# Kernel tuning notes

Hardware: AMD Instinct MI355X
Metric: run time of the kernel (lower is better)

Reference implementation:

```python
import jax, jax.numpy as jnp
import numpy as np

N, E = 20000, 320000
IN_DIM = OUT_DIM = E_IN = E_OUT = 128
BN_EPS = 1e-5

def _lrelu(x):
    return jnp.where(x >= 0, x, 0.1 * x)

def setup_inputs() -> dict:
    key = jax.random.key(0)
    ks = jax.random.split(key, 12)
    def w(k, shape):
        return jax.random.normal(k, shape, jnp.float32) * (shape[0] ** -0.5)
    return {
        "h": jax.random.normal(ks[0], (N, IN_DIM), jnp.float32),
        "edge_w": jax.random.normal(ks[1], (E, E_IN), jnp.float32),
        "W_node": w(ks[2], (IN_DIM, OUT_DIM)),
        "W_eedge": w(ks[3], (E_IN, E_IN)),
        "W_esf": w(ks[4], (E_IN, 1)),
        "W_fuse": w(ks[5], (2 * OUT_DIM + E_IN, OUT_DIM)),
        "b_fuse": jnp.zeros((OUT_DIM,), jnp.float32),
        "W_attn": w(ks[6], (OUT_DIM, 1)),
        "W_conc": w(ks[7], (2 * OUT_DIM + E_IN, OUT_DIM)),
        "b_conc": jnp.zeros((OUT_DIM,), jnp.float32),
        "bn_gamma": jnp.ones((E_IN,), jnp.float32),
        "bn_beta": jnp.zeros((E_IN,), jnp.float32),
        "W_aggre": w(ks[8], (2 * OUT_DIM + 2 * E_IN, E_OUT)),
        "src": jax.random.randint(ks[9], (E,), 0, N),
        "dst": jax.random.randint(ks[10], (E,), 0, N),
    }

def reference(h, edge_w, W_node, W_eedge, W_esf, W_fuse, b_fuse, W_attn,
              W_conc, b_conc, bn_gamma, bn_beta, W_aggre, src, dst):
    # eval mode: dropout = identity, BatchNorm uses running stats (mean 0, var 1)
    hn = h @ W_node                       # embed_node -> ndata['h'] = ndata['oh']
    # self_attention: ow = embed_edge(w); w = edge_sf_atten(lrelu(ow)) * ow
    ow = edge_w @ W_eedge                 # [E, e_in]
    w1 = (_lrelu(ow) @ W_esf) * ow        # [E, e_in]
    # inter_attention
    hs, hd = hn[src], hn[dst]             # [E, out]
    sat = jnp.concatenate([hs, hd, w1], axis=-1)          # [E, 2*out+e_in]
    inw = _lrelu(sat @ W_fuse + b_fuse)                   # [E, out]
    a = inw @ W_attn                                      # [E, 1]
    w2 = a * w1                                           # edata['w']
    # reduce_func2: segment softmax over incoming edges (grouped by dst)
    s = a[:, 0]
    m = jax.ops.segment_max(s, dst, num_segments=N)
    e = jnp.exp(s - m[dst])
    denom = jax.ops.segment_sum(e, dst, num_segments=N)
    alpha = (e / denom[dst])[:, None]                     # [E, 1]
    t = jnp.concatenate([hs, w2], axis=-1)                # [E, out+e_in]
    h_agg = jax.ops.segment_sum(alpha * t, dst, num_segments=N)  # [N, out+e_in]
    h_new = jnp.concatenate([h_agg, hn], axis=-1) @ W_conc + b_conc
    # DGL only updates nodes that received messages; zero-indegree keep embed_node(h)
    indeg = jax.ops.segment_sum(jnp.ones((E,), jnp.float32), dst, num_segments=N)
    h_out = jnp.where(indeg[:, None] > 0, h_new, hn)      # [N, out]
    # edge_calc: BN(w2) then aggre_embed_edge(cat(src_h, dst_h, bn_w, ow))
    w_bn = (w2 / jnp.sqrt(jnp.float32(1.0) + BN_EPS)) * bn_gamma + bn_beta
    z = jnp.concatenate([h_out[src], h_out[dst], w_bn, ow], axis=-1)
    w_out = z @ W_aggre                                   # [E, e_out]
    return h_out, w_out, sat
```

## Files before the change

kernel.cpp:

```cpp
#include <hip/hip_runtime.h>
#include <hip/hip_bf16.h>

#define TB 256
#define TBM 512
#define BM 64
#define BK 32
#define BN 128
#define ASTR 68
#define MAXD 160

static constexpr int NN = 20000;
static constexpr int NE = 320000;

static constexpr long long OFF_HN   = 0;
static constexpr long long OFF_OW   = 2560000;
static constexpr long long OFF_S    = 43520000;
static constexpr long long OFF_DEN  = 43840000;
static constexpr long long OFF_CUR  = 43860000;
static constexpr long long OFF_HAGG = 43880000;
static constexpr long long OFF_WT   = 49000000;
static constexpr long long WS_FLOATS = 49140000;

static constexpr int U_E = 0;
static constexpr int U_F = 32768;
static constexpr int U_A = 131072;

static constexpr long long OUT_HOUT = 0;
static constexpr long long OUT_WOUT = 2560000;
static constexpr long long OUT_SAT  = 43520000;

typedef __attribute__((ext_vector_type(8))) short s8v;
typedef __attribute__((ext_vector_type(4))) float f32x4;
typedef __attribute__((ext_vector_type(4))) unsigned short u16x4;

#define MFMA16(a,b,c) __builtin_amdgcn_mfma_f32_16x16x32_bf16(a,b,c,0,0,0)

__device__ __forceinline__ float lrelu(float x){ return x >= 0.f ? x : 0.1f*x; }

__device__ __forceinline__ void gl16(const void* g, void* l){
    __builtin_amdgcn_global_load_lds(
        (const __attribute__((address_space(1))) void*)g,
        (__attribute__((address_space(3))) void*)l, 16, 0, 0);
}

__device__ __forceinline__ void split1(float f, unsigned short& hi, unsigned short& lo){
    __hip_bfloat16 h = __float2bfloat16(f);
    float hf = __bfloat162float(h);
    __hip_bfloat16 l = __float2bfloat16(f - hf);
    hi = __builtin_bit_cast(unsigned short, h);
    lo = __builtin_bit_cast(unsigned short, l);
}
__device__ __forceinline__ void split8(float4 a, float4 b, s8v& hi, s8v& lo){
    float v[8] = {a.x,a.y,a.z,a.w,b.x,b.y,b.z,b.w};
#pragma unroll
    for (int j = 0; j < 8; ++j){
        unsigned short hs, ls;
        split1(v[j], hs, ls);
        hi[j] = (short)hs; lo[j] = (short)ls;
    }
}
__device__ __forceinline__ float bfp(unsigned p){
    return __uint_as_float(p & 0xffff0000u) + __uint_as_float(p << 16);
}

__device__ __forceinline__ int lds_a(int row, int g){
    return row*32 + ((g ^ (row & 3)) << 3);
}

__device__ __forceinline__ void store_At(float (*Ast)[ASTR], int k4, int r, float4 v){
    Ast[k4+0][r] = v.x; Ast[k4+1][r] = v.y; Ast[k4+2][r] = v.z; Ast[k4+3][r] = v.w;
}
__device__ __forceinline__ void mm_chunk(const float (*Ast)[ASTR], const float (*Bs)[BN],
                                         int r0, int c0, float acc[4][8]){
#pragma unroll 4
    for (int k = 0; k < BK; ++k){
        const float4 av = *(const float4*)&Ast[k][r0];
        const float4 b0 = *(const float4*)&Bs[k][c0];
        const float4 b1 = *(const float4*)&Bs[k][64 + c0];
        const float a0=av.x, a1=av.y, a2=av.z, a3=av.w;
        const float b[8] = {b0.x,b0.y,b0.z,b0.w,b1.x,b1.y,b1.z,b1.w};
#pragma unroll
        for (int j = 0; j < 8; ++j){
            acc[0][j] = fmaf(a0, b[j], acc[0][j]);
            acc[1][j] = fmaf(a1, b[j], acc[1][j]);
            acc[2][j] = fmaf(a2, b[j], acc[2][j]);
            acc[3][j] = fmaf(a3, b[j], acc[3][j]);
        }
    }
}
__device__ __forceinline__ void load_B(const float* __restrict__ W, int kc,
                                       float (*Bs)[BN], int tid){
#pragma unroll
    for (int p = 0; p < 4; ++p){
        int idx = p*TB + tid;
        int row = idx >> 5;
        int c4  = (idx & 31) << 2;
        *(float4*)&Bs[row][c4] = *(const float4*)&W[(size_t)(kc+row)*BN + c4];
    }
}

__global__ __launch_bounds__(TB) void k_prep(const float* __restrict__ We,
                                             const float* __restrict__ Wf,
                                             const float* __restrict__ Wa,
                                             unsigned short* __restrict__ wt,
                                             int* __restrict__ cur){
    int id = blockIdx.x*TB + threadIdx.x;
    if (id < NN) cur[id] = 0;
    unsigned short hs, ls;
    if (id < 16384){
        int n = id >> 7, k = id & 127;
        split1(We[(size_t)k*128 + n], hs, ls);
        wt[U_E + id] = hs; wt[U_E + 16384 + id] = ls;
    } else if (id < 65536){
        int local = id - 16384;
        int n = local / 384, k = local - n*384;
        split1(Wf[(size_t)k*128 + n], hs, ls);
        wt[U_F + local] = hs; wt[U_F + 49152 + local] = ls;
    } else if (id < 131072){
        int local = id - 65536;
        int n = local >> 9, k = local & 511;
        split1(Wa[(size_t)k*128 + n], hs, ls);
        wt[U_A + local] = hs; wt[U_A + 65536 + local] = ls;
    }
}

__global__ __launch_bounds__(TB) void kB_count(const int* __restrict__ dst,
                                               int* __restrict__ cur){
    int e = blockIdx.x*TB + threadIdx.x;
    atomicAdd(&cur[dst[e]], 1);
}
__global__ __launch_bounds__(TB) void kC_scan(int* __restrict__ cur,
                                              int* __restrict__ offs){
    __shared__ int part[TB];
    __shared__ int spre[TB];
    const int tid = threadIdx.x;
    const int CH = (NN + TB - 1) / TB;
    const int base = tid * CH;
    int sum = 0;
    for (int i = 0; i < CH; ++i){ int idx = base + i; if (idx < NN) sum += cur[idx]; }
    part[tid] = sum;
    __syncthreads();
    if (tid == 0){ int r = 0; for (int i = 0; i < TB; ++i){ spre[i] = r; r += part[i]; } }
    __syncthreads();
    int run = spre[tid];
    for (int i = 0; i < CH; ++i){
        int idx = base + i;
        if (idx < NN){ int c = cur[idx]; offs[idx] = run; cur[idx] = run; run += c; }
    }
}
__global__ __launch_bounds__(TB) void kD_scatter(const int* __restrict__ dst,
                                                 int* __restrict__ cur,
                                                 int* __restrict__ eidx){
    int e = blockIdx.x*TB + threadIdx.x;
    int p = atomicAdd(&cur[dst[e]], 1);
    eidx[p] = e;
}

__global__ __launch_bounds__(TB) void k1_hn(const float* __restrict__ h,
                                            const float* __restrict__ Wn,
                                            unsigned short* __restrict__ hnH,
                                            unsigned short* __restrict__ hnL,
                                            unsigned* __restrict__ hnP){
    __shared__ float Ast[BK][ASTR];
    __shared__ float Bs[BK][BN];
    const int tid = threadIdx.x;
    const int rbase = blockIdx.x * BM;
    const int tc = tid & 15, tr = tid >> 4;
    const int r0 = tr*4, c0 = tc*4;
    float acc[4][8] = {};
    for (int kc = 0; kc < 128; kc += BK){
        __syncthreads();
        {
            int lr = tid >> 3, k4 = (tid & 7) << 2;
#pragma unroll
            for (int p = 0; p < 2; ++p){
                int r = p*32 + lr;
                int rr = rbase + r; if (rr >= NN) rr = NN-1;
                float4 v = *(const float4*)&h[(size_t)rr*128 + kc + k4];
                store_At(Ast, k4, r, v);
            }
        }
        load_B(Wn, kc, Bs, tid);
        __syncthreads();
        mm_chunk(Ast, Bs, r0, c0, acc);
    }
#pragma unroll
    for (int i = 0; i < 4; ++i){
        int rr = rbase + r0 + i;
        if (rr < NN){
            u16x4 h0, l0, h1, l1;
            uint4 p0, p1;
#pragma unroll
            for (int j = 0; j < 4; ++j){
                unsigned short hs, ls;
                split1(acc[i][j], hs, ls);
                h0[j] = hs; l0[j] = ls;
                ((unsigned*)&p0)[j] = ((unsigned)hs << 16) | ls;
                split1(acc[i][4+j], hs, ls);
                h1[j] = hs; l1[j] = ls;
                ((unsigned*)&p1)[j] = ((unsigned)hs << 16) | ls;
            }
            *(u16x4*)&hnH[(size_t)rr*128 + c0] = h0;
            *(u16x4*)&hnL[(size_t)rr*128 + c0] = l0;
            *(u16x4*)&hnH[(size_t)rr*128 + 64 + c0] = h1;
            *(u16x4*)&hnL[(size_t)rr*128 + 64 + c0] = l1;
            *(uint4*)&hnP[(size_t)rr*128 + c0] = p0;
            *(uint4*)&hnP[(size_t)rr*128 + 64 + c0] = p1;
        }
    }
}


__global__ __launch_bounds__(TBM) void k2_mfma(const float* __restrict__ ew,
                                               const unsigned short* __restrict__ wtH,
                                               const unsigned short* __restrict__ wtL,
                                               const float* __restrict__ Wesf,
                                               unsigned short* __restrict__ owH,
                                               unsigned short* __restrict__ owL,
                                               float* __restrict__ sat){
    __shared__ __align__(16) unsigned short Ah[2][4096], Al[2][4096], Bh[2][4096], Bl[2][4096];
    __shared__ float sEsf[128];
    const int tid = threadIdx.x;
    const long long rbase = (long long)blockIdx.x * 128;
    const int lane = tid & 63, w = tid >> 6;
    const int ls = lane & 15, lg = lane >> 4;
    const int srow = tid >> 2, sg = tid & 3;
    const int gsw = sg ^ (srow & 3);
    const int aslot = srow*32 + (gsw << 3);
    if (tid < 128) sEsf[tid] = Wesf[tid];
    f32x4 acc[8] = {};
    auto stage = [&](int nb, int t){
        const int kc = t*32;
        gl16(&wtH[srow*128 + kc + gsw*8], &Bh[nb][w*512]);
        gl16(&wtL[srow*128 + kc + gsw*8], &Bl[nb][w*512]);
        const float* p = &ew[(rbase + srow)*128 + kc + sg*8];
        float4 v0 = *(const float4*)p, v1 = *(const float4*)(p+4);
        s8v hi, lo; split8(v0, v1, hi, lo);
        *(s8v*)&Ah[nb][aslot] = hi; *(s8v*)&Al[nb][aslot] = lo;
    };
    stage(0, 0);
    __syncthreads();
    int cur = 0;
    for (int t = 0; t < 4; ++t){
        if (t+1 < 4) stage(cur^1, t+1);
        s8v ah = *(const s8v*)&Ah[cur][lds_a(w*16 + ls, lg)];
        s8v al = *(const s8v*)&Al[cur][lds_a(w*16 + ls, lg)];
#pragma unroll
        for (int ct = 0; ct < 8; ++ct){
            int c = ct*16 + ls;
            s8v bh = *(const s8v*)&Bh[cur][lds_a(c,lg)];
            s8v bl = *(const s8v*)&Bl[cur][lds_a(c,lg)];
            acc[ct] = MFMA16(ah, bh, acc[ct]);
            acc[ct] = MFMA16(ah, bl, acc[ct]);
            acc[ct] = MFMA16(al, bh, acc[ct]);
        }
        __syncthreads();
        cur ^= 1;
    }
#pragma unroll
    for (int reg = 0; reg < 4; ++reg){
        float p = 0.f;
#pragma unroll
        for (int ct = 0; ct < 8; ++ct)
            p += lrelu(acc[ct][reg]) * sEsf[ct*16 + ls];
#pragma unroll
        for (int m = 1; m < 16; m <<= 1) p += __shfl_xor(p, m);
        long long orow = rbase + w*16 + lg*4 + reg;
#pragma unroll
        for (int ct = 0; ct < 8; ++ct){
            float o = acc[ct][reg];
            int col = ct*16 + ls;
            sat[orow*384 + 256 + col] = p * o;
            unsigned short hs_, ls_; split1(o, hs_, ls_);
            owH[orow*128 + col] = hs_;
            owL[orow*128 + col] = ls_;
        }
    }
}

__global__ __launch_bounds__(TBM) void k3_mfma(const unsigned short* __restrict__ hnH,
                                               const unsigned short* __restrict__ hnL,
                                               const unsigned* __restrict__ hnP,
                                               const unsigned short* __restrict__ wtH,
                                               const unsigned short* __restrict__ wtL,
                                               const float* __restrict__ bf,
                                               const float* __restrict__ Wattn,
                                               const int* __restrict__ src,
                                               const int* __restrict__ dst,
                                               float* __restrict__ sat,
                                               float* __restrict__ s_ws){
    __shared__ __align__(16) unsigned short Ah[2][4096], Al[2][4096], Bh[2][4096], Bl[2][4096];
    __shared__ float sBf[128], sAtt[128];
    __shared__ int sSrc[128], sDst[128];
    const int tid = threadIdx.x;
    const long long rbase = (long long)blockIdx.x * 128;
    const int lane = tid & 63, w = tid >> 6;
    const int ls = lane & 15, lg = lane >> 4;
    const int srow = tid >> 2, sg = tid & 3;
    const int gsw = sg ^ (srow & 3);
    const int aslot = srow*32 + (gsw << 3);
    if (tid < 128){
        sBf[tid] = bf[tid]; sAtt[tid] = Wattn[tid];
        sSrc[tid] = src[rbase + tid]; sDst[tid] = dst[rbase + tid];
    }
    __syncthreads();
    f32x4 acc[8] = {};
    auto stage = [&](int nb, int t){
        const int kc = t*32;
        gl16(&wtH[srow*384 + kc + gsw*8], &Bh[nb][w*512]);
        gl16(&wtL[srow*384 + kc + gsw*8], &Bl[nb][w*512]);
        long long e = rbase + srow;
        if (kc < 256){
            int node = (kc < 128) ? sSrc[srow] : sDst[srow];
            int col0 = kc & 127;
            gl16(&hnH[(size_t)node*128 + col0 + gsw*8], &Ah[nb][w*512]);
            gl16(&hnL[(size_t)node*128 + col0 + gsw*8], &Al[nb][w*512]);
            const unsigned* pp = &hnP[(size_t)node*128 + col0 + sg*8];
            uint4 q0 = *(const uint4*)pp, q1 = *(const uint4*)(pp+4);
            float4 v0 = {bfp(q0.x), bfp(q0.y), bfp(q0.z), bfp(q0.w)};
            float4 v1 = {bfp(q1.x), bfp(q1.y), bfp(q1.z), bfp(q1.w)};
            *(float4*)&sat[e*384 + kc + sg*8] = v0;
            *(float4*)&sat[e*384 + kc + sg*8 + 4] = v1;
        } else {
            const float* p = &sat[e*384 + kc + sg*8];
            float4 v0 = *(const float4*)p, v1 = *(const float4*)(p+4);
            s8v hi, lo; split8(v0, v1, hi, lo);
            *(s8v*)&Ah[nb][aslot] = hi; *(s8v*)&Al[nb][aslot] = lo;
        }
    };
    stage(0, 0);
    __syncthreads();
    int cur = 0;
    for (int t = 0; t < 12; ++t){
        if (t+1 < 12) stage(cur^1, t+1);
        s8v ah = *(const s8v*)&Ah[cur][lds_a(w*16 + ls, lg)];
        s8v al = *(const s8v*)&Al[cur][lds_a(w*16 + ls, lg)];
#pragma unroll
        for (int ct = 0; ct < 8; ++ct){
            int c = ct*16 + ls;
            s8v bh = *(const s8v*)&Bh[cur][lds_a(c,lg)];
            s8v bl = *(const s8v*)&Bl[cur][lds_a(c,lg)];
            acc[ct] = MFMA16(ah, bh, acc[ct]);
            acc[ct] = MFMA16(ah, bl, acc[ct]);
            acc[ct] = MFMA16(al, bh, acc[ct]);
        }
        __syncthreads();
        cur ^= 1;
    }
#pragma unroll
    for (int reg = 0; reg < 4; ++reg){
        float p = 0.f;
#pragma unroll
        for (int ct = 0; ct < 8; ++ct){
            int col = ct*16 + ls;
            p += lrelu(acc[ct][reg] + sBf[col]) * sAtt[col];
        }
#pragma unroll
        for (int m = 1; m < 16; m <<= 1) p += __shfl_xor(p, m);
        if (ls == 0) s_ws[rbase + w*16 + lg*4 + reg] = p;
    }
}

__global__ __launch_bounds__(TB) void k5_agg(const float* __restrict__ s,
                                             const unsigned* __restrict__ hnP,
                                             const float* __restrict__ sat,
                                             const int* __restrict__ src,
                                             const int* __restrict__ eidx,
                                             const int* __restrict__ offs,
                                             const int* __restrict__ cur,
                                             float* __restrict__ hagg,
                                             float* __restrict__ den){
    __shared__ int   sEu[4][MAXD];
    __shared__ int   sEs[4][MAXD];
    __shared__ float sAl[4][MAXD];
    __shared__ float sWc[4][MAXD];
    const int wv = threadIdx.x >> 6, lane = threadIdx.x & 63;
    const int n = blockIdx.x*4 + wv;
    int* Eu = sEu[wv]; int* Es = sEs[wv];
    float* Al = sAl[wv]; float* Wc = sWc[wv];
    const int start = offs[n];
    const int deg = cur[n] - start;
    const int dc = deg < MAXD ? deg : MAXD;
    for (int i = lane; i < dc; i += 64) Eu[i] = eidx[start+i];
    __syncthreads();
    for (int i = lane; i < dc; i += 64){
        int my = Eu[i], r = 0;
        for (int j = 0; j < dc; ++j) r += (Eu[j] < my);
        Es[r] = my;
    }
    __syncthreads();
    float lm = -3.402823466e38f;
    for (int i = lane; i < dc; i += 64){
        int e = Es[i];
        float sv = s[e];
        Wc[i] = sv;
        Eu[i] = src[e];
        lm = fmaxf(lm, sv);
    }
    for (int i = MAXD + lane; i < deg; i += 64) lm = fmaxf(lm, s[eidx[start+i]]);
#pragma unroll
    for (int m2 = 32; m2; m2 >>= 1) lm = fmaxf(lm, __shfl_xor(lm, m2));
    const float m = lm;
    float lsum = 0.f;
    for (int i = lane; i < dc; i += 64){
        float ev = expf(Wc[i] - m);
        Al[i] = ev;
        lsum += ev;
    }
    for (int i = MAXD + lane; i < deg; i += 64) lsum += expf(s[eidx[start+i]] - m);
#pragma unroll
    for (int m2 = 32; m2; m2 >>= 1) lsum += __shfl_xor(lsum, m2);
    const float denom = lsum;
    const float inv = (deg > 0) ? 1.f/denom : 0.f;
    for (int i = lane; i < dc; i += 64){
        float al = Al[i] * inv;
        Al[i] = al;
        Wc[i] = al * Wc[i];
    }
    __syncthreads();
    float a0=0.f, a1=0.f, a2=0.f, a3=0.f;
    for (int i = 0; i < dc; ++i){
        int sI = Eu[i];
        size_t e = (size_t)Es[i];
        float al = Al[i], wc = Wc[i];
        unsigned p0 = hnP[(size_t)sI*128 + lane];
        unsigned p1 = hnP[(size_t)sI*128 + 64 + lane];
        float w0 = sat[e*384 + 256 + lane];
        float w1v = sat[e*384 + 256 + 64 + lane];
        a0 = fmaf(al, bfp(p0), a0);
        a1 = fmaf(al, bfp(p1), a1);
        a2 = fmaf(wc, w0, a2);
        a3 = fmaf(wc, w1v, a3);
    }
    for (int i = MAXD; i < deg; ++i){
        int e = eidx[start+i];
        float sv = s[e];
        float al = expf(sv - m) * inv;
        float wc = al * sv;
        int sI = src[e];
        a0 = fmaf(al, bfp(hnP[(size_t)sI*128 + lane]), a0);
        a1 = fmaf(al, bfp(hnP[(size_t)sI*128 + 64 + lane]), a1);
        a2 = fmaf(wc, sat[(size_t)e*384 + 256 + lane], a2);
        a3 = fmaf(wc, sat[(size_t)e*384 + 256 + 64 + lane], a3);
    }
    const size_t b = (size_t)n*256;
    hagg[b + lane] = a0;
    hagg[b + 64 + lane] = a1;
    hagg[b + 128 + lane] = a2;
    hagg[b + 192 + lane] = a3;
    if (lane == 0) den[n] = (deg > 0) ? denom : 0.f;
}

__global__ __launch_bounds__(TB) void k6_conc(const float* hagg,
                                              const unsigned* __restrict__ hnP,
                                              const float* __restrict__ Wc,
                                              const float* __restrict__ bc,
                                              const float* __restrict__ den,
                                              float* __restrict__ hout,
                                              unsigned short* houtHL){
    __shared__ float Ast[BK][ASTR];
    __shared__ float Bs[BK][BN];
    __shared__ float sBc[BN];
    const int tid = threadIdx.x;
    const int rbase = blockIdx.x * BM;
    const int tc = tid & 15, tr = tid >> 4;
    const int r0 = tr*4, c0 = tc*4;
    if (tid < BN) sBc[tid] = bc[tid];
    float acc[4][8] = {};
    for (int chunk = 0; chunk < 12; ++chunk){
        int kc = chunk * BK;
        __syncthreads();
        {
            int lr = tid >> 3, k4 = (tid & 7) << 2;
#pragma unroll
            for (int p = 0; p < 2; ++p){
                int r = p*32 + lr;
                int rr = rbase + r; if (rr >= NN) rr = NN-1;
                float4 v;
                if (chunk < 8) v = *(const float4*)&hagg[(size_t)rr*256 + kc + k4];
                else {
                    int cb = (kc - 256) + k4;
                    uint4 q = *(const uint4*)&hnP[(size_t)rr*128 + cb];
                    v.x = bfp(q.x); v.y = bfp(q.y); v.z = bfp(q.z); v.w = bfp(q.w);
                }
                store_At(Ast, k4, r, v);
            }
        }
        load_B(Wc, kc, Bs, tid);
        __syncthreads();
        mm_chunk(Ast, Bs, r0, c0, acc);
    }
#pragma unroll
    for (int i = 0; i < 4; ++i){
        int rr = rbase + r0 + i;
        if (rr >= NN) continue;
        bool keep = den[rr] > 0.f;
        float o[8];
#pragma unroll
        for (int j = 0; j < 8; ++j){
            int col = (j < 4) ? (c0 + j) : (60 + c0 + j);
            float fb = bfp(hnP[(size_t)rr*128 + col]);
            o[j] = keep ? acc[i][j] + sBc[col] : fb;
        }
        float4 o0 = {o[0],o[1],o[2],o[3]}, o1 = {o[4],o[5],o[6],o[7]};
        *(float4*)&hout[(size_t)rr*128 + c0] = o0;
        *(float4*)&hout[(size_t)rr*128 + 64 + c0] = o1;
        u16x4 h0, l0, h1, l1;
#pragma unroll
        for (int j = 0; j < 4; ++j){
            unsigned short hs, ls2;
            split1(o[j], hs, ls2);   h0[j] = hs; l0[j] = ls2;
            split1(o[4+j], hs, ls2); h1[j] = hs; l1[j] = ls2;
        }
        *(u16x4*)&houtHL[(size_t)rr*512 + c0] = h0;
        *(u16x4*)&houtHL[(size_t)rr*512 + 128 + c0] = l0;
        *(u16x4*)&houtHL[(size_t)rr*512 + 64 + c0] = h1;
        *(u16x4*)&houtHL[(size_t)rr*512 + 128 + 64 + c0] = l1;
    }
}

__global__ __launch_bounds__(TBM) void k7_mfma(const unsigned short* __restrict__ houtHL,
                                               const unsigned short* __restrict__ owH,
                                               const unsigned short* __restrict__ owL,
                                               const float* __restrict__ sarr,
                                               const float* __restrict__ sat,
                                               const float* __restrict__ gamma,
                                               const float* __restrict__ beta,
                                               const unsigned short* __restrict__ wtH,
                                               const unsigned short* __restrict__ wtL,
                                               const int* __restrict__ src,
                                               const int* __restrict__ dst,
                                               float* __restrict__ w2out){
    __shared__ __align__(16) unsigned short Ah[2][4096], Al[2][4096], Bh[2][4096], Bl[2][4096];
    __shared__ float sGam[128], sBet[128], sS[128];
    __shared__ int sSrc[128], sDst[128];
    const int tid = threadIdx.x;
    const long long rbase = (long long)blockIdx.x * 128;
    const int lane = tid & 63, w = tid >> 6;
    const int ls = lane & 15, lg = lane >> 4;
    const int srow = tid >> 2, sg = tid & 3;
    const int gsw = sg ^ (srow & 3);
    const int aslot = srow*32 + (gsw << 3);
    const float ISR = 0.9999950000374997f;
    if (tid < 128){
        sGam[tid] = gamma[tid] * ISR; sBet[tid] = beta[tid];
        sSrc[tid] = src[rbase + tid]; sDst[tid] = dst[rbase + tid];
        sS[tid] = sarr[rbase + tid];
    }
    __syncthreads();
    f32x4 acc[8] = {};
    auto stage = [&](int nb, int t){
        const int kc = t*32;
        gl16(&wtH[srow*512 + kc + gsw*8], &Bh[nb][w*512]);
        gl16(&wtL[srow*512 + kc + gsw*8], &Bl[nb][w*512]);
        long long e = rbase + srow;
        if (kc < 256){
            int node = (kc < 128) ? sSrc[srow] : sDst[srow];
            int col0 = kc & 127;
            gl16(&houtHL[(size_t)node*512 + col0 + gsw*8], &Ah[nb][w*512]);
            gl16(&houtHL[(size_t)node*512 + 128 + col0 + gsw*8], &Al[nb][w*512]);
        } else if (kc < 384){
            int cb = (kc - 256) + sg*8;
            float se = sS[srow];
            const float* p = &sat[e*384 + 256 + cb];
            float4 v0 = *(const float4*)p, v1 = *(const float4*)(p+4);
            v0.x = fmaf(v0.x*se, sGam[cb+0], sBet[cb+0]);
            v0.y = fmaf(v0.y*se, sGam[cb+1], sBet[cb+1]);
            v0.z = fmaf(v0.z*se, sGam[cb+2], sBet[cb+2]);
            v0.w = fmaf(v0.w*se, sGam[cb+3], sBet[cb+3]);
            v1.x = fmaf(v1.x*se, sGam[cb+4], sBet[cb+4]);
            v1.y = fmaf(v1.y*se, sGam[cb+5], sBet[cb+5]);
            v1.z = fmaf(v1.z*se, sGam[cb+6], sBet[cb+6]);
            v1.w = fmaf(v1.w*se, sGam[cb+7], sBet[cb+7]);
            s8v hi, lo; split8(v0, v1, hi, lo);
            *(s8v*)&Ah[nb][aslot] = hi; *(s8v*)&Al[nb][aslot] = lo;
        } else {
            int col0 = kc - 384;
            gl16(&owH[e*128 + col0 + gsw*8], &Ah[nb][w*512]);
            gl16(&owL[e*128 + col0 + gsw*8], &Al[nb][w*512]);
        }
    };
    stage(0, 0);
    __syncthreads();
    int cur = 0;
    for (int t = 0; t < 16; ++t){
        if (t+1 < 16) stage(cur^1, t+1);
        s8v ah = *(const s8v*)&Ah[cur][lds_a(w*16 + ls, lg)];
        s8v al = *(const s8v*)&Al[cur][lds_a(w*16 + ls, lg)];
#pragma unroll
        for (int ct = 0; ct < 8; ++ct){
            int c = ct*16 + ls;
            s8v bh = *(const s8v*)&Bh[cur][lds_a(c,lg)];
            s8v bl = *(const s8v*)&Bl[cur][lds_a(c,lg)];
            acc[ct] = MFMA16(ah, bh, acc[ct]);
            acc[ct] = MFMA16(ah, bl, acc[ct]);
            acc[ct] = MFMA16(al, bh, acc[ct]);
        }
        __syncthreads();
        cur ^= 1;
    }
#pragma unroll
    for (int reg = 0; reg < 4; ++reg){
        long long orow = rbase + w*16 + lg*4 + reg;
#pragma unroll
        for (int ct = 0; ct < 8; ++ct)
            w2out[orow*128 + ct*16 + ls] = acc[ct][reg];
    }
}

extern "C" void kernel_launch(void* const* d_in, const int* in_sizes, int n_in,
                              void* d_out, int out_size, void* d_ws, size_t ws_size,
                              hipStream_t stream){
    (void)in_sizes; (void)n_in; (void)out_size;
    const float* h       = (const float*)d_in[0];
    const float* edge_w  = (const float*)d_in[1];
    const float* W_node  = (const float*)d_in[2];
    const float* W_eedge = (const float*)d_in[3];
    const float* W_esf   = (const float*)d_in[4];
    const float* W_fuse  = (const float*)d_in[5];
    const float* b_fuse  = (const float*)d_in[6];
    const float* W_attn  = (const float*)d_in[7];
    const float* W_conc  = (const float*)d_in[8];
    const float* b_conc  = (const float*)d_in[9];
    const float* gamma   = (const float*)d_in[10];
    const float* beta    = (const float*)d_in[11];
    const float* W_aggre = (const float*)d_in[12];
    const int*   src     = (const int*)d_in[13];
    const int*   dst     = (const int*)d_in[14];

    float* out    = (float*)d_out;
    float* o_hout = out + OUT_HOUT;
    float* o_wout = out + OUT_WOUT;
    float* o_sat  = out + OUT_SAT;

    if (ws_size < (size_t)WS_FLOATS * 4) return;
    float* ws     = (float*)d_ws;
    unsigned short* w_hnH = (unsigned short*)(ws + OFF_HN);
    unsigned short* w_hnL = w_hnH + (size_t)NN*128;
    unsigned short* w_owH = (unsigned short*)(ws + OFF_OW);
    unsigned short* w_owL = w_owH + (size_t)NE*128;
    float* w_s    = ws + OFF_S;
    float* w_den  = ws + OFF_DEN;
    int*   w_cur  = (int*)(ws + OFF_CUR);
    float* w_hagg = ws + OFF_HAGG;
    unsigned short* w_houtHL = (unsigned short*)w_hagg;
    unsigned short* w_wt = (unsigned short*)(ws + OFF_WT);

    unsigned* w_hnP = (unsigned*)o_wout;
    int* w_eidx = (int*)o_hout;
    int* w_offs = w_eidx + NE;

    hipLaunchKernelGGL(k_prep,    dim3(131072/TB), dim3(TB), 0, stream,
                       W_eedge, W_fuse, W_aggre, w_wt, w_cur);
    hipLaunchKernelGGL(kB_count,  dim3(NE/TB), dim3(TB), 0, stream, dst, w_cur);
    hipLaunchKernelGGL(kC_scan,   dim3(1), dim3(TB), 0, stream, w_cur, w_offs);
    hipLaunchKernelGGL(kD_scatter,dim3(NE/TB), dim3(TB), 0, stream, dst, w_cur, w_eidx);
    hipLaunchKernelGGL(k1_hn,     dim3((NN+BM-1)/BM), dim3(TB), 0, stream, h, W_node,
                       w_hnH, w_hnL, w_hnP);
    hipLaunchKernelGGL(k2_mfma,   dim3(NE/128), dim3(TBM), 0, stream, edge_w,
                       w_wt + U_E, w_wt + U_E + 128*128, W_esf,
                       w_owH, w_owL, o_sat);
    hipLaunchKernelGGL(k3_mfma,   dim3(NE/128), dim3(TBM), 0, stream, w_hnH, w_hnL, w_hnP,
                       w_wt + U_F, w_wt + U_F + 128*384, b_fuse, W_attn,
                       src, dst, o_sat, w_s);
    hipLaunchKernelGGL(k5_agg,    dim3(NN/4), dim3(TB), 0, stream, w_s, w_hnP, o_sat,
                       src, w_eidx, w_offs, w_cur, w_hagg, w_den);
    hipLaunchKernelGGL(k6_conc,   dim3((NN+BM-1)/BM), dim3(TB), 0, stream, w_hagg,
                       w_hnP, W_conc, b_conc, w_den, o_hout, w_houtHL);
    hipLaunchKernelGGL(k7_mfma,   dim3(NE/128), dim3(TBM), 0, stream, w_houtHL,
                       w_owH, w_owL, w_s, o_sat, gamma, beta,
                       w_wt + U_A, w_wt + U_A + 128*512,
                       src, dst, o_wout);
}
```

Measured before the change: 711.5 us.

## Precompute per-node projections to shrink edge GEMMs and fold edge weight chain

Uses linearity to move the hs/hd parts of the fuse and aggre GEMMs from per-edge to per-node: a new node GEMM computes hn@W_fuse[0:256] and h_out@W_aggre[0:256] once per node, and edge kernels gather and add these rows instead of multiplying gathered features. The w1 contribution to the fuse layer is folded into a combined W_eedge@W_fuse3 weight so the edge-embedding and fuse GEMMs merge into one 256-wide kernel. This cuts edge GEMM K from 384/512 to 128/256 and removes a kernel plus the hn hi/lo buffers. In exchange it adds extra gathers and small node GEMMs, and changes rounding order because of the reassociation.

```diff
diff --git a/kernel.cpp b/kernel.cpp
--- a/kernel.cpp
+++ b/kernel.cpp
@@ -11,19 +11,21 @@
 
 static constexpr int NN = 20000;
 static constexpr int NE = 320000;
-
-static constexpr long long OFF_HN   = 0;
-static constexpr long long OFF_OW   = 2560000;
-static constexpr long long OFF_S    = 43520000;
-static constexpr long long OFF_DEN  = 43840000;
-static constexpr long long OFF_CUR  = 43860000;
-static constexpr long long OFF_HAGG = 43880000;
-static constexpr long long OFF_WT   = 49000000;
-static constexpr long long WS_FLOATS = 49140000;
-
-static constexpr int U_E = 0;
-static constexpr int U_F = 32768;
-static constexpr int U_A = 131072;
+static constexpr int NB = 313;
+
+static constexpr long long OFF_OW  = 0;
+static constexpr long long OFF_PQ  = 40960000;
+static constexpr long long OFF_S   = 46080000;
+static constexpr long long OFF_DEN = 46400000;
+static constexpr long long OFF_CUR = 46420000;
+static constexpr long long OFF_WT  = 46440000;
+static constexpr long long OFF_C2  = 46505536;
+static constexpr long long WS_FLOATS = 46525000;
+
+static constexpr int U_E2H = 0;
+static constexpr int U_E2L = 32768;
+static constexpr int U_A2H = 65536;
+static constexpr int U_A2L = 98304;
 
 static constexpr long long OUT_HOUT = 0;
 static constexpr long long OUT_WOUT = 2560000;
@@ -31,7 +33,6 @@
 
 typedef __attribute__((ext_vector_type(8))) short s8v;
 typedef __attribute__((ext_vector_type(4))) float f32x4;
-typedef __attribute__((ext_vector_type(4))) unsigned short u16x4;
 
 #define MFMA16(a,b,c) __builtin_amdgcn_mfma_f32_16x16x32_bf16(a,b,c,0,0,0)
 
@@ -61,10 +62,6 @@
 }
 __device__ __forceinline__ float bfp(unsigned p){
     return __uint_as_float(p & 0xffff0000u) + __uint_as_float(p << 16);
-}
-
-__device__ __forceinline__ int lds_a(int row, int g){
-    return row*32 + ((g ^ (row & 3)) << 3);
 }
 
 __device__ __forceinline__ void store_At(float (*Ast)[ASTR], int k4, int r, float4 v){
@@ -99,28 +96,59 @@
     }
 }
 
-__global__ __launch_bounds__(TB) void k_prep(const float* __restrict__ We,
-                                             const float* __restrict__ Wf,
-                                             const float* __restrict__ Wa,
-                                             unsigned short* __restrict__ wt,
-                                             int* __restrict__ cur){
+__global__ __launch_bounds__(TB) void kC2(const float* __restrict__ We,
+                                          const float* __restrict__ Wf3,
+                                          float* __restrict__ C2){
+    __shared__ float Ast[BK][ASTR];
+    __shared__ float Bs[BK][BN];
+    const int tid = threadIdx.x;
+    const int rbase = blockIdx.x * BM;
+    const int tc = tid & 15, tr = tid >> 4;
+    const int r0 = tr*4, c0 = tc*4;
+    float acc[4][8] = {};
+    for (int kc = 0; kc < 128; kc += BK){
+        __syncthreads();
+        {
+            int lr = tid >> 3, k4 = (tid & 7) << 2;
+#pragma unroll
+            for (int p = 0; p < 2; ++p){
+                int r = p*32 + lr;
+                float4 v = *(const float4*)&We[(size_t)(rbase+r)*128 + kc + k4];
+                store_At(Ast, k4, r, v);
+            }
+        }
+        load_B(Wf3, kc, Bs, tid);
+        __syncthreads();
+        mm_chunk(Ast, Bs, r0, c0, acc);
+    }
+#pragma unroll
+    for (int i = 0; i < 4; ++i){
+        int rr = rbase + r0 + i;
+        float4 o0 = {acc[i][0],acc[i][1],acc[i][2],acc[i][3]};
+        float4 o1 = {acc[i][4],acc[i][5],acc[i][6],acc[i][7]};
+        *(float4*)&C2[(size_t)rr*128 + c0] = o0;
+        *(float4*)&C2[(size_t)rr*128 + 64 + c0] = o1;
+    }
+}
+
+__global__ __launch_bounds__(TB) void kP2(const float* __restrict__ We,
+                                          const float* __restrict__ C2,
+                                          const float* __restrict__ Wa,
+                                          unsigned short* __restrict__ wt,
+                                          int* __restrict__ cur){
     int id = blockIdx.x*TB + threadIdx.x;
     if (id < NN) cur[id] = 0;
     unsigned short hs, ls;
-    if (id < 16384){
-        int n = id >> 7, k = id & 127;
-        split1(We[(size_t)k*128 + n], hs, ls);
-        wt[U_E + id] = hs; wt[U_E + 16384 + id] = ls;
+    if (id < 32768){
+        int col = id >> 7, k = id & 127;
+        float v = (col < 128) ? We[(size_t)k*128 + col] : C2[(size_t)k*128 + (col-128)];
+        split1(v, hs, ls);
+        wt[U_E2H + id] = hs; wt[U_E2L + id] = ls;
     } else if (id < 65536){
-        int local = id - 16384;
-        int n = local / 384, k = local - n*384;
-        split1(Wf[(size_t)k*128 + n], hs, ls);
-        wt[U_F + local] = hs; wt[U_F + 49152 + local] = ls;
-    } else if (id < 131072){
-        int local = id - 65536;
-        int n = local >> 9, k = local & 511;
-        split1(Wa[(size_t)k*128 + n], hs, ls);
-        wt[U_A + local] = hs; wt[U_A + 65536 + local] = ls;
+        int local = id - 32768;
+        int col = local >> 8, kk = local & 255;
+        split1(Wa[(size_t)(256+kk)*128 + col], hs, ls);
+        wt[U_A2H + local] = hs; wt[U_A2L + local] = ls;
     }
 }
 
@@ -158,8 +186,6 @@
 
 __global__ __launch_bounds__(TB) void k1_hn(const float* __restrict__ h,
                                             const float* __restrict__ Wn,
-                                            unsigned short* __restrict__ hnH,
-                                            unsigned short* __restrict__ hnL,
                                             unsigned* __restrict__ hnP){
     __shared__ float Ast[BK][ASTR];
     __shared__ float Bs[BK][BN];
@@ -188,177 +214,221 @@
     for (int i = 0; i < 4; ++i){
         int rr = rbase + r0 + i;
         if (rr < NN){
-            u16x4 h0, l0, h1, l1;
             uint4 p0, p1;
 #pragma unroll
             for (int j = 0; j < 4; ++j){
                 unsigned short hs, ls;
                 split1(acc[i][j], hs, ls);
-                h0[j] = hs; l0[j] = ls;
                 ((unsigned*)&p0)[j] = ((unsigned)hs << 16) | ls;
                 split1(acc[i][4+j], hs, ls);
-                h1[j] = hs; l1[j] = ls;
                 ((unsigned*)&p1)[j] = ((unsigned)hs << 16) | ls;
             }
-            *(u16x4*)&hnH[(size_t)rr*128 + c0] = h0;
-            *(u16x4*)&hnL[(size_t)rr*128 + c0] = l0;
-            *(u16x4*)&hnH[(size_t)rr*128 + 64 + c0] = h1;
-            *(u16x4*)&hnL[(size_t)rr*128 + 64 + c0] = l1;
             *(uint4*)&hnP[(size_t)rr*128 + c0] = p0;
             *(uint4*)&hnP[(size_t)rr*128 + 64 + c0] = p1;
         }
     }
 }
 
-
-__global__ __launch_bounds__(TBM) void k2_mfma(const float* __restrict__ ew,
+__global__ __launch_bounds__(TB) void kNG(const unsigned* __restrict__ aP,
+                                          const float* __restrict__ aF,
+                                          int packed,
+                                          const float* __restrict__ W,
+                                          float* __restrict__ O){
+    __shared__ float Ast[BK][ASTR];
+    __shared__ float Bs[BK][BN];
+    const int tid = threadIdx.x;
+    const int half = blockIdx.x >= NB ? 1 : 0;
+    const int rbase = (blockIdx.x - half*NB) * BM;
+    const float* Wp = W + (size_t)half*16384;
+    const int tc = tid & 15, tr = tid >> 4;
+    const int r0 = tr*4, c0 = tc*4;
+    float acc[4][8] = {};
+    for (int kc = 0; kc < 128; kc += BK){
+        __syncthreads();
+        {
+            int lr = tid >> 3, k4 = (tid & 7) << 2;
+#pragma unroll
+            for (int p = 0; p < 2; ++p){
+                int r = p*32 + lr;
+                int rr = rbase + r; if (rr >= NN) rr = NN-1;
+                float4 v;
+                if (packed){
+                    uint4 q = *(const uint4*)&aP[(size_t)rr*128 + kc + k4];
+                    v.x = bfp(q.x); v.y = bfp(q.y); v.z = bfp(q.z); v.w = bfp(q.w);
+                } else {
+                    v = *(const float4*)&aF[(size_t)rr*128 + kc + k4];
+                }
+                store_At(Ast, k4, r, v);
+            }
+        }
+        load_B(Wp, kc, Bs, tid);
+        __syncthreads();
+        mm_chunk(Ast, Bs, r0, c0, acc);
+    }
+#pragma unroll
+    for (int i = 0; i < 4; ++i){
+        int rr = rbase + r0 + i;
+        if (rr < NN){
+            float4 o0 = {acc[i][0],acc[i][1],acc[i][2],acc[i][3]};
+            float4 o1 = {acc[i][4],acc[i][5],acc[i][6],acc[i][7]};
+            *(float4*)&O[(size_t)rr*256 + half*128 + c0] = o0;
+            *(float4*)&O[(size_t)rr*256 + half*128 + 64 + c0] = o1;
+        }
+    }
+}
+
+__global__ __launch_bounds__(TBM) void k2_mega(const float* __restrict__ ew,
                                                const unsigned short* __restrict__ wtH,
                                                const unsigned short* __restrict__ wtL,
                                                const float* __restrict__ Wesf,
+                                               const float* __restrict__ Wattn,
+                                               const float* __restrict__ bf,
+                                               const float* __restrict__ P,
+                                               const unsigned* __restrict__ hnP,
+                                               const int* __restrict__ src,
+                                               const int* __restrict__ dst,
                                                unsigned short* __restrict__ owH,
                                                unsigned short* __restrict__ owL,
-                                               float* __restrict__ sat){
-    __shared__ __align__(16) unsigned short Ah[2][4096], Al[2][4096], Bh[2][4096], Bl[2][4096];
-    __shared__ float sEsf[128];
+                                               float* __restrict__ sat,
+                                               float* __restrict__ s_ws){
+    __shared__ __align__(16) unsigned short Ah[2][2048], Al[2][2048];
+    __shared__ __align__(16) unsigned short Bh[2][8192], Bl[2][8192];
+    float* eEsf = (float*)&Ah[0][0];
+    float* eAtt = eEsf + 128;
+    float* eBf  = eAtt + 128;
+    float* ePl  = eBf + 128;
+    float* eSl  = ePl + 128;
+    int*   eSrc = (int*)(eSl + 128);
+    int*   eDst = eSrc + 64;
     const int tid = threadIdx.x;
-    const long long rbase = (long long)blockIdx.x * 128;
+    const long long rbase = (long long)blockIdx.x * 64;
     const int lane = tid & 63, w = tid >> 6;
     const int ls = lane & 15, lg = lane >> 4;
-    const int srow = tid >> 2, sg = tid & 3;
-    const int gsw = sg ^ (srow & 3);
-    const int aslot = srow*32 + (gsw << 3);
-    if (tid < 128) sEsf[tid] = Wesf[tid];
-    f32x4 acc[8] = {};
+    const int rgrp = w & 1, cg = w >> 1;
+    f32x4 acc[2][4] = {};
     auto stage = [&](int nb, int t){
         const int kc = t*32;
-        gl16(&wtH[srow*128 + kc + gsw*8], &Bh[nb][w*512]);
-        gl16(&wtL[srow*128 + kc + gsw*8], &Bl[nb][w*512]);
-        const float* p = &ew[(rbase + srow)*128 + kc + sg*8];
-        float4 v0 = *(const float4*)p, v1 = *(const float4*)(p+4);
-        s8v hi, lo; split8(v0, v1, hi, lo);
-        *(s8v*)&Ah[nb][aslot] = hi; *(s8v*)&Al[nb][aslot] = lo;
+#pragma unroll
+        for (int q = 0; q < 2; ++q){
+            int col = q*128 + w*16 + (lane>>2);
+            int g = (lane&3) ^ (col&3);
+            gl16(&wtH[col*128 + kc + g*8], &Bh[nb][q*4096 + w*512]);
+            gl16(&wtL[col*128 + kc + g*8], &Bl[nb][q*4096 + w*512]);
+        }
+        if (tid < 256){
+            int srow = tid >> 2, sg = tid & 3;
+            const float* p = &ew[(rbase + srow)*128 + kc + sg*8];
+            float4 v0 = *(const float4*)p, v1 = *(const float4*)(p+4);
+            s8v hi, lo; split8(v0, v1, hi, lo);
+            int slot = srow*32 + ((sg ^ (srow&3)) << 3);
+            *(s8v*)&Ah[nb][slot] = hi; *(s8v*)&Al[nb][slot] = lo;
+        }
     };
     stage(0, 0);
     __syncthreads();
     int cur = 0;
     for (int t = 0; t < 4; ++t){
         if (t+1 < 4) stage(cur^1, t+1);
-        s8v ah = *(const s8v*)&Ah[cur][lds_a(w*16 + ls, lg)];
-        s8v al = *(const s8v*)&Al[cur][lds_a(w*16 + ls, lg)];
-#pragma unroll
-        for (int ct = 0; ct < 8; ++ct){
-            int c = ct*16 + ls;
-            s8v bh = *(const s8v*)&Bh[cur][lds_a(c,lg)];
-            s8v bl = *(const s8v*)&Bl[cur][lds_a(c,lg)];
-            acc[ct] = MFMA16(ah, bh, acc[ct]);
-            acc[ct] = MFMA16(ah, bl, acc[ct]);
-            acc[ct] = MFMA16(al, bh, acc[ct]);
+        s8v ah[2], al[2];
+#pragma unroll
+        for (int rt = 0; rt < 2; ++rt){
+            int r = rgrp*32 + rt*16 + ls;
+            int idx = r*32 + ((lg ^ (r&3)) << 3);
+            ah[rt] = *(const s8v*)&Ah[cur][idx];
+            al[rt] = *(const s8v*)&Al[cur][idx];
+        }
+#pragma unroll
+        for (int ct = 0; ct < 4; ++ct){
+            int c = cg*64 + ct*16 + ls;
+            int idx = c*32 + ((lg ^ (c&3)) << 3);
+            s8v bh = *(const s8v*)&Bh[cur][idx];
+            s8v bl = *(const s8v*)&Bl[cur][idx];
+#pragma unroll
+            for (int rt = 0; rt < 2; ++rt){
+                acc[rt][ct] = MFMA16(ah[rt], bh, acc[rt][ct]);
+                acc[rt][ct] = MFMA16(ah[rt], bl, acc[rt][ct]);
+                acc[rt][ct] = MFMA16(al[rt], bh, acc[rt][ct]);
+            }
         }
         __syncthreads();
         cur ^= 1;
     }
-#pragma unroll
-    for (int reg = 0; reg < 4; ++reg){
-        float p = 0.f;
-#pragma unroll
-        for (int ct = 0; ct < 8; ++ct)
-            p += lrelu(acc[ct][reg]) * sEsf[ct*16 + ls];
-#pragma unroll
-        for (int m = 1; m < 16; m <<= 1) p += __shfl_xor(p, m);
-        long long orow = rbase + w*16 + lg*4 + reg;
-#pragma unroll
-        for (int ct = 0; ct < 8; ++ct){
-            float o = acc[ct][reg];
-            int col = ct*16 + ls;
-            sat[orow*384 + 256 + col] = p * o;
-            unsigned short hs_, ls_; split1(o, hs_, ls_);
-            owH[orow*128 + col] = hs_;
-            owL[orow*128 + col] = ls_;
-        }
-    }
-}
-
-__global__ __launch_bounds__(TBM) void k3_mfma(const unsigned short* __restrict__ hnH,
-                                               const unsigned short* __restrict__ hnL,
-                                               const unsigned* __restrict__ hnP,
-                                               const unsigned short* __restrict__ wtH,
-                                               const unsigned short* __restrict__ wtL,
-                                               const float* __restrict__ bf,
-                                               const float* __restrict__ Wattn,
-                                               const int* __restrict__ src,
-                                               const int* __restrict__ dst,
-                                               float* __restrict__ sat,
-                                               float* __restrict__ s_ws){
-    __shared__ __align__(16) unsigned short Ah[2][4096], Al[2][4096], Bh[2][4096], Bl[2][4096];
-    __shared__ float sBf[128], sAtt[128];
-    __shared__ int sSrc[128], sDst[128];
-    const int tid = threadIdx.x;
-    const long long rbase = (long long)blockIdx.x * 128;
-    const int lane = tid & 63, w = tid >> 6;
-    const int ls = lane & 15, lg = lane >> 4;
-    const int srow = tid >> 2, sg = tid & 3;
-    const int gsw = sg ^ (srow & 3);
-    const int aslot = srow*32 + (gsw << 3);
-    if (tid < 128){
-        sBf[tid] = bf[tid]; sAtt[tid] = Wattn[tid];
-        sSrc[tid] = src[rbase + tid]; sDst[tid] = dst[rbase + tid];
-    }
-    __syncthreads();
-    f32x4 acc[8] = {};
-    auto stage = [&](int nb, int t){
-        const int kc = t*32;
-        gl16(&wtH[srow*384 + kc + gsw*8], &Bh[nb][w*512]);
-        gl16(&wtL[srow*384 + kc + gsw*8], &Bl[nb][w*512]);
-        long long e = rbase + srow;
-        if (kc < 256){
-            int node = (kc < 128) ? sSrc[srow] : sDst[srow];
-            int col0 = kc & 127;
-            gl16(&hnH[(size_t)node*128 + col0 + gsw*8], &Ah[nb][w*512]);
-            gl16(&hnL[(size_t)node*128 + col0 + gsw*8], &Al[nb][w*512]);
-            const unsigned* pp = &hnP[(size_t)node*128 + col0 + sg*8];
-            uint4 q0 = *(const uint4*)pp, q1 = *(const uint4*)(pp+4);
-            float4 v0 = {bfp(q0.x), bfp(q0.y), bfp(q0.z), bfp(q0.w)};
-            float4 v1 = {bfp(q1.x), bfp(q1.y), bfp(q1.z), bfp(q1.w)};
-            *(float4*)&sat[e*384 + kc + sg*8] = v0;
-            *(float4*)&sat[e*384 + kc + sg*8 + 4] = v1;
-        } else {
-            const float* p = &sat[e*384 + kc + sg*8];
-            float4 v0 = *(const float4*)p, v1 = *(const float4*)(p+4);
-            s8v hi, lo; split8(v0, v1, hi, lo);
-            *(s8v*)&Ah[nb][aslot] = hi; *(s8v*)&Al[nb][aslot] = lo;
-        }
-    };
-    stage(0, 0);
-    __syncthreads();
-    int cur = 0;
-    for (int t = 0; t < 12; ++t){
-        if (t+1 < 12) stage(cur^1, t+1);
-        s8v ah = *(const s8v*)&Ah[cur][lds_a(w*16 + ls, lg)];
-        s8v al = *(const s8v*)&Al[cur][lds_a(w*16 + ls, lg)];
-#pragma unroll
-        for (int ct = 0; ct < 8; ++ct){
-            int c = ct*16 + ls;
-            s8v bh = *(const s8v*)&Bh[cur][lds_a(c,lg)];
-            s8v bl = *(const s8v*)&Bl[cur][lds_a(c,lg)];
-            acc[ct] = MFMA16(ah, bh, acc[ct]);
-            acc[ct] = MFMA16(ah, bl, acc[ct]);
-            acc[ct] = MFMA16(al, bh, acc[ct]);
-        }
-        __syncthreads();
-        cur ^= 1;
-    }
-#pragma unroll
-    for (int reg = 0; reg < 4; ++reg){
-        float p = 0.f;
-#pragma unroll
-        for (int ct = 0; ct < 8; ++ct){
-            int col = ct*16 + ls;
-            p += lrelu(acc[ct][reg] + sBf[col]) * sAtt[col];
-        }
-#pragma unroll
-        for (int m = 1; m < 16; m <<= 1) p += __shfl_xor(p, m);
-        if (ls == 0) s_ws[rbase + w*16 + lg*4 + reg] = p;
-    }
+    if (tid < 128){ eEsf[tid] = Wesf[tid]; eAtt[tid] = Wattn[tid]; eBf[tid] = bf[tid]; }
+    if (tid < 64){ eSrc[tid] = src[rbase + tid]; eDst[tid] = dst[rbase + tid]; }
+    __syncthreads();
+    if (cg < 2){
+#pragma unroll
+        for (int rt = 0; rt < 2; ++rt){
+#pragma unroll
+            for (int reg = 0; reg < 4; ++reg){
+                float pp = 0.f;
+#pragma unroll
+                for (int ct = 0; ct < 4; ++ct){
+                    int col = cg*64 + ct*16 + ls;
+                    pp += lrelu(acc[rt][ct][reg]) * eEsf[col];
+                }
+#pragma unroll
+                for (int m = 1; m < 16; m <<= 1) pp += __shfl_xor(pp, m);
+                int row = rgrp*32 + rt*16 + lg*4 + reg;
+                if (ls == 0) ePl[row*2 + cg] = pp;
+            }
+        }
+    } else {
+        int wv = w - 4;
+        for (int i = lane; i < 1024; i += 64){
+            int row = wv*16 + (i >> 6), q = i & 63;
+            int node = (q < 32) ? eSrc[row] : eDst[row];
+            uint4 pv = *(const uint4*)&hnP[(size_t)node*128 + ((q & 31) << 2)];
+            float4 v = {bfp(pv.x), bfp(pv.y), bfp(pv.z), bfp(pv.w)};
+            *(float4*)&sat[(rbase + row)*384 + q*4] = v;
+        }
+    }
+    __syncthreads();
+    if (cg < 2){
+#pragma unroll
+        for (int rt = 0; rt < 2; ++rt){
+#pragma unroll
+            for (int reg = 0; reg < 4; ++reg){
+                int row = rgrp*32 + rt*16 + lg*4 + reg;
+                float pr = ePl[row*2] + ePl[row*2 + 1];
+                long long orow = rbase + row;
+#pragma unroll
+                for (int ct = 0; ct < 4; ++ct){
+                    int col = cg*64 + ct*16 + ls;
+                    float o = acc[rt][ct][reg];
+                    sat[orow*384 + 256 + col] = pr * o;
+                    unsigned short hs_, ls_; split1(o, hs_, ls_);
+                    owH[orow*128 + col] = hs_;
+                    owL[orow*128 + col] = ls_;
+                }
+            }
+        }
+    } else {
+#pragma unroll
+        for (int rt = 0; rt < 2; ++rt){
+#pragma unroll
+            for (int reg = 0; reg < 4; ++reg){
+                int row = rgrp*32 + rt*16 + lg*4 + reg;
+                float pr = ePl[row*2] + ePl[row*2 + 1];
+                int sI = eSrc[row], dI = eDst[row];
+                float sp = 0.f;
+#pragma unroll
+                for (int ct = 0; ct < 4; ++ct){
+                    int c = (cg-2)*64 + ct*16 + ls;
+                    float val = pr * acc[rt][ct][reg]
+                              + P[(size_t)sI*256 + c]
+                              + P[(size_t)dI*256 + 128 + c]
+                              + eBf[c];
+                    sp += lrelu(val) * eAtt[c];
+                }
+#pragma unroll
+                for (int m = 1; m < 16; m <<= 1) sp += __shfl_xor(sp, m);
+                if (ls == 0) eSl[row*2 + (cg-2)] = sp;
+            }
+        }
+    }
+    __syncthreads();
+    if (tid < 64) s_ws[rbase + tid] = eSl[tid*2] + eSl[tid*2 + 1];
 }
 
 __global__ __launch_bounds__(TB) void k5_agg(const float* __restrict__ s,
@@ -451,13 +521,12 @@
     if (lane == 0) den[n] = (deg > 0) ? denom : 0.f;
 }
 
-__global__ __launch_bounds__(TB) void k6_conc(const float* hagg,
+__global__ __launch_bounds__(TB) void k6_conc(const float* __restrict__ hagg,
                                               const unsigned* __restrict__ hnP,
                                               const float* __restrict__ Wc,
                                               const float* __restrict__ bc,
                                               const float* __restrict__ den,
-                                              float* __restrict__ hout,
-                                              unsigned short* houtHL){
+                                              float* __restrict__ hout){
     __shared__ float Ast[BK][ASTR];
     __shared__ float Bs[BK][BN];
     __shared__ float sBc[BN];
@@ -505,32 +574,21 @@
         float4 o0 = {o[0],o[1],o[2],o[3]}, o1 = {o[4],o[5],o[6],o[7]};
         *(float4*)&hout[(size_t)rr*128 + c0] = o0;
         *(float4*)&hout[(size_t)rr*128 + 64 + c0] = o1;
-        u16x4 h0, l0, h1, l1;
-#pragma unroll
-        for (int j = 0; j < 4; ++j){
-            unsigned short hs, ls2;
-            split1(o[j], hs, ls2);   h0[j] = hs; l0[j] = ls2;
-            split1(o[4+j], hs, ls2); h1[j] = hs; l1[j] = ls2;
-        }
-        *(u16x4*)&houtHL[(size_t)rr*512 + c0] = h0;
-        *(u16x4*)&houtHL[(size_t)rr*512 + 128 + c0] = l0;
-        *(u16x4*)&houtHL[(size_t)rr*512 + 64 + c0] = h1;
-        *(u16x4*)&houtHL[(size_t)rr*512 + 128 + 64 + c0] = l1;
-    }
-}
-
-__global__ __launch_bounds__(TBM) void k7_mfma(const unsigned short* __restrict__ houtHL,
-                                               const unsigned short* __restrict__ owH,
-                                               const unsigned short* __restrict__ owL,
-                                               const float* __restrict__ sarr,
-                                               const float* __restrict__ sat,
-                                               const float* __restrict__ gamma,
-                                               const float* __restrict__ beta,
-                                               const unsigned short* __restrict__ wtH,
-                                               const unsigned short* __restrict__ wtL,
-                                               const int* __restrict__ src,
-                                               const int* __restrict__ dst,
-                                               float* __restrict__ w2out){
+    }
+}
+
+__global__ __launch_bounds__(TBM) void k7p(const unsigned short* __restrict__ owH,
+                                           const unsigned short* __restrict__ owL,
+                                           const float* __restrict__ sarr,
+                                           const float* __restrict__ sat,
+                                           const float* __restrict__ Q,
+                                           const float* __restrict__ gamma,
+                                           const float* __restrict__ beta,
+                                           const unsigned short* __restrict__ wtH,
+                                           const unsigned short* __restrict__ wtL,
+                                           const int* __restrict__ src,
+                                           const int* __restrict__ dst,
+                                           float* __restrict__ w2out){
     __shared__ __align__(16) unsigned short Ah[2][4096], Al[2][4096], Bh[2][4096], Bl[2][4096];
     __shared__ float sGam[128], sBet[128], sS[128];
     __shared__ int sSrc[128], sDst[128];
@@ -551,16 +609,11 @@
     f32x4 acc[8] = {};
     auto stage = [&](int nb, int t){
         const int kc = t*32;
-        gl16(&wtH[srow*512 + kc + gsw*8], &Bh[nb][w*512]);
-        gl16(&wtL[srow*512 + kc + gsw*8], &Bl[nb][w*512]);
+        gl16(&wtH[srow*256 + kc + gsw*8], &Bh[nb][w*512]);
+        gl16(&wtL[srow*256 + kc + gsw*8], &Bl[nb][w*512]);
         long long e = rbase + srow;
-        if (kc < 256){
-            int node = (kc < 128) ? sSrc[srow] : sDst[srow];
-            int col0 = kc & 127;
-            gl16(&houtHL[(size_t)node*512 + col0 + gsw*8], &Ah[nb][w*512]);
-            gl16(&houtHL[(size_t)node*512 + 128 + col0 + gsw*8], &Al[nb][w*512]);
-        } else if (kc < 384){
-            int cb = (kc - 256) + sg*8;
+        if (kc < 128){
+            int cb = kc + sg*8;
             float se = sS[srow];
             const float* p = &sat[e*384 + 256 + cb];
             float4 v0 = *(const float4*)p, v1 = *(const float4*)(p+4);
@@ -575,7 +628,7 @@
             s8v hi, lo; split8(v0, v1, hi, lo);
             *(s8v*)&Ah[nb][aslot] = hi; *(s8v*)&Al[nb][aslot] = lo;
         } else {
-            int col0 = kc - 384;
+            int col0 = kc - 128;
             gl16(&owH[e*128 + col0 + gsw*8], &Ah[nb][w*512]);
             gl16(&owL[e*128 + col0 + gsw*8], &Al[nb][w*512]);
         }
@@ -583,15 +636,16 @@
     stage(0, 0);
     __syncthreads();
     int cur = 0;
-    for (int t = 0; t < 16; ++t){
-        if (t+1 < 16) stage(cur^1, t+1);
-        s8v ah = *(const s8v*)&Ah[cur][lds_a(w*16 + ls, lg)];
-        s8v al = *(const s8v*)&Al[cur][lds_a(w*16 + ls, lg)];
+    for (int t = 0; t < 8; ++t){
+        if (t+1 < 8) stage(cur^1, t+1);
+        int r = w*16 + ls;
+        s8v ah = *(const s8v*)&Ah[cur][r*32 + ((lg ^ (r&3)) << 3)];
+        s8v al = *(const s8v*)&Al[cur][r*32 + ((lg ^ (r&3)) << 3)];
 #pragma unroll
         for (int ct = 0; ct < 8; ++ct){
             int c = ct*16 + ls;
-            s8v bh = *(const s8v*)&Bh[cur][lds_a(c,lg)];
-            s8v bl = *(const s8v*)&Bl[cur][lds_a(c,lg)];
+            s8v bh = *(const s8v*)&Bh[cur][c*32 + ((lg ^ (c&3)) << 3)];
+            s8v bl = *(const s8v*)&Bl[cur][c*32 + ((lg ^ (c&3)) << 3)];
             acc[ct] = MFMA16(ah, bh, acc[ct]);
             acc[ct] = MFMA16(ah, bl, acc[ct]);
             acc[ct] = MFMA16(al, bh, acc[ct]);
@@ -601,10 +655,16 @@
     }
 #pragma unroll
     for (int reg = 0; reg < 4; ++reg){
-        long long orow = rbase + w*16 + lg*4 + reg;
-#pragma unroll
-        for (int ct = 0; ct < 8; ++ct)
-            w2out[orow*128 + ct*16 + ls] = acc[ct][reg];
+        int row = w*16 + lg*4 + reg;
+        long long orow = rbase + row;
+        int sI = sSrc[row], dI = sDst[row];
+#pragma unroll
+        for (int ct = 0; ct < 8; ++ct){
+            int col = ct*16 + ls;
+            w2out[orow*128 + col] = acc[ct][reg]
+                                  + Q[(size_t)sI*256 + col]
+                                  + Q[(size_t)dI*256 + 128 + col];
+        }
     }
 }
 
@@ -635,40 +695,39 @@
 
     if (ws_size < (size_t)WS_FLOATS * 4) return;
     float* ws     = (float*)d_ws;
-    unsigned short* w_hnH = (unsigned short*)(ws + OFF_HN);
-    unsigned short* w_hnL = w_hnH + (size_t)NN*128;
     unsigned short* w_owH = (unsigned short*)(ws + OFF_OW);
     unsigned short* w_owL = w_owH + (size_t)NE*128;
+    float* w_PQ   = ws + OFF_PQ;
     float* w_s    = ws + OFF_S;
     float* w_den  = ws + OFF_DEN;
     int*   w_cur  = (int*)(ws + OFF_CUR);
-    float* w_hagg = ws + OFF_HAGG;
-    unsigned short* w_houtHL = (unsigned short*)w_hagg;
     unsigned short* w_wt = (unsigned short*)(ws + OFF_WT);
+    float* w_C2   = ws + OFF_C2;
 
     unsigned* w_hnP = (unsigned*)o_wout;
     int* w_eidx = (int*)o_hout;
     int* w_offs = w_eidx + NE;
 
-    hipLaunchKernelGGL(k_prep,    dim3(131072/TB), dim3(TB), 0, stream,
-                       W_eedge, W_fuse, W_aggre, w_wt, w_cur);
+    hipLaunchKernelGGL(kC2,       dim3(2), dim3(TB), 0, stream,
+                       W_eedge, W_fuse + (size_t)256*128, w_C2);
+    hipLaunchKernelGGL(kP2,       dim3(65536/TB), dim3(TB), 0, stream,
+                       W_eedge, w_C2, W_aggre, w_wt, w_cur);
     hipLaunchKernelGGL(kB_count,  dim3(NE/TB), dim3(TB), 0, stream, dst, w_cur);
     hipLaunchKernelGGL(kC_scan,   dim3(1), dim3(TB), 0, stream, w_cur, w_offs);
     hipLaunchKernelGGL(kD_scatter,dim3(NE/TB), dim3(TB), 0, stream, dst, w_cur, w_eidx);
-    hipLaunchKernelGGL(k1_hn,     dim3((NN+BM-1)/BM), dim3(TB), 0, stream, h, W_node,
-                       w_hnH, w_hnL, w_hnP);
-    hipLaunchKernelGGL(k2_mfma,   dim3(NE/128), dim3(TBM), 0, stream, edge_w,
-                       w_wt + U_E, w_wt + U_E + 128*128, W_esf,
-                       w_owH, w_owL, o_sat);
-    hipLaunchKernelGGL(k3_mfma,   dim3(NE/128), dim3(TBM), 0, stream, w_hnH, w_hnL, w_hnP,
-                       w_wt + U_F, w_wt + U_F + 128*384, b_fuse, W_attn,
-                       src, dst, o_sat, w_s);
+    hipLaunchKernelGGL(k1_hn,     dim3(NB), dim3(TB), 0, stream, h, W_node, w_hnP);
+    hipLaunchKernelGGL(kNG,       dim3(2*NB), dim3(TB), 0, stream,
+                       w_hnP, (const float*)nullptr, 1, W_fuse, w_PQ);
+    hipLaunchKernelGGL(k2_mega,   dim3(NE/64), dim3(TBM), 0, stream, edge_w,
+                       w_wt + U_E2H, w_wt + U_E2L, W_esf, W_attn, b_fuse,
+                       w_PQ, w_hnP, src, dst, w_owH, w_owL, o_sat, w_s);
     hipLaunchKernelGGL(k5_agg,    dim3(NN/4), dim3(TB), 0, stream, w_s, w_hnP, o_sat,
-                       src, w_eidx, w_offs, w_cur, w_hagg, w_den);
-    hipLaunchKernelGGL(k6_conc,   dim3((NN+BM-1)/BM), dim3(TB), 0, stream, w_hagg,
-                       w_hnP, W_conc, b_conc, w_den, o_hout, w_houtHL);
-    hipLaunchKernelGGL(k7_mfma,   dim3(NE/128), dim3(TBM), 0, stream, w_houtHL,
-                       w_owH, w_owL, w_s, o_sat, gamma, beta,
-                       w_wt + U_A, w_wt + U_A + 128*512,
-                       src, dst, o_wout);
-}
+                       src, w_eidx, w_offs, w_cur, w_PQ, w_den);
+    hipLaunchKernelGGL(k6_conc,   dim3(NB), dim3(TB), 0, stream, w_PQ,
+                       w_hnP, W_conc, b_conc, w_den, o_hout);
+    hipLaunchKernelGGL(kNG,       dim3(2*NB), dim3(TB), 0, stream,
+                       (const unsigned*)nullptr, o_hout, 0, W_aggre, w_PQ);
+    hipLaunchKernelGGL(k7p,       dim3(NE/128), dim3(TBM), 0, stream,
+                       w_owH, w_owL, w_s, o_sat, w_PQ, gamma, beta,
+                       w_wt + U_A2H, w_wt + U_A2L, src, dst, o_wout);
+}
```

Measured after the change: 762.9 us. 7.2% more time.
